# Kernel tuning notes

Measured on AMD Instinct MI355X. Metric: run time of the kernel, lower is better.

## Reference

```python
import jax, jax.numpy as jnp
import numpy as np

B = 524288
IN_DIM = 16
OUT_DIM = 32  # hidden_dim3
N_CHUNKS = 4
CHUNK = 4


def ste_round(x):
    # straight-through round (grad passes unchanged, like Round.apply)
    return x + jax.lax.stop_gradient(jnp.round(x) - x)


def ste_sign(x):
    # straight-through sign (grad passes unchanged, like Sign.apply)
    return x + jax.lax.stop_gradient(jnp.sign(x) - x)


def setup_inputs() -> dict:
    key = jax.random.key(0)
    k1, k2 = jax.random.split(key)
    Input = jax.random.uniform(k1, (B, IN_DIM), dtype=jnp.float32)
    weight = jax.random.normal(k2, (OUT_DIM, IN_DIM), dtype=jnp.float32)
    InMin = jnp.float32(0.0)
    InMax = jnp.float32(1.0)
    return {"Input": Input, "weight": weight, "InMin": InMin, "InMax": InMax}


def reference(Input, weight, InMin, InMax):
    # eval-mode forward of QuantLinear
    scale = InMax - InMin
    w = ste_sign(weight)                       # [O, I] in {-1, 0, 1}
    wP = jax.nn.relu(w)                        # positive mask
    wM = jax.nn.relu(-w)                       # negative mask

    # 4-bit input quantization (eval path): clip(round((x-min)/(max-min)*15), 0, 15)
    q = jnp.clip(ste_round((Input - InMin) / scale * 15.0), 0.0, 15.0)  # [B, I]

    # bias = linear(InMin * ones, w): each row = InMin * sum_j w[o, j]
    bias = InMin * jnp.sum(w, axis=1)          # [O], broadcasts over batch

    # chunked 4-wide linears, vectorized over the 4 chunks
    qc = q.reshape(B, N_CHUNKS, CHUNK)         # [B, C, 4]
    wPc = wP.reshape(OUT_DIM, N_CHUNKS, CHUNK)  # [O, C, 4]
    wMc = wM.reshape(OUT_DIM, N_CHUNKS, CHUNK)
    yP = jnp.einsum('bcf,ocf->cbo', qc, wPc)   # [C, B, O]
    yM = jnp.einsum('bcf,ocf->cbo', qc, wMc)   # [C, B, O]

    # accumulate clip(round(y/15), -4, 4) * (InMax - InMin) over all 8 terms
    terms = jnp.clip(ste_round(yP / 15.0), -4.0, 4.0) \
          + jnp.clip(ste_round(-yM / 15.0), -4.0, 4.0)  # [C, B, O]
    x = jnp.sum(terms, axis=0) * scale + bias  # [B, O]
    return x
```

## Files before the change

### kernel.cpp

```cpp
#include <hip/hip_runtime.h>
#include <stdint.h>


#if __has_builtin(__builtin_amdgcn_sdot4)
#define HAVE_SDOT4 1
#else
#define HAVE_SDOT4 0
#endif

__device__ __forceinline__ int dot7(uint32_t q, uint32_t m) {
#if HAVE_SDOT4
    return __builtin_amdgcn_sdot4((int)q, (int)m, 7, false);
#else
    return (int)(((q & m) * 0x01010101u) >> 24) + 7;
#endif
}

__device__ __forceinline__ int r15(int y7) {
    return (int)(((uint32_t)y7 * 274u) >> 12);
}

__global__ __launch_bounds__(256) void qlin_kernel(
    const float* __restrict__ in, const float* __restrict__ wgt,
    const float* __restrict__ pmin, const float* __restrict__ pmax,
    float* __restrict__ out, int nrows)
{
    __shared__ uint4 smask[64];
    __shared__ __align__(16) float sbias[32];

    const int t = threadIdx.x;
    const int lane = t & 63;
    const int wave = (blockIdx.x << 2) + (t >> 6);
    const size_t R0 = (size_t)wave * 64;

    const float4* inp = (const float4*)in + R0 * 4 + lane;
    float4 f0, f1, f2, f3;
    const bool live = (long)R0 < (long)nrows;
    if (live) {
        f0 = inp[0];
        f1 = inp[64];
        f2 = inp[128];
        f3 = inp[192];
    }

    const float InMin = pmin[0];
    const float InMax = pmax[0];
    const float scale = __fsub_rn(InMax, InMin);

    const uint32_t MASKBYTE = HAVE_SDOT4 ? 1u : 0xFFu;

    {
        int o = t >> 3, k = t & 7, c = k & 3, isM = k >> 2;
        const float* wrow = wgt + o * 16 + c * 4;
        uint32_t m = 0;
#pragma unroll
        for (int j = 0; j < 4; ++j) {
            float v = wrow[j];
            bool sel = isM ? (v < 0.0f) : (v > 0.0f);
            if (sel) m |= MASKBYTE << (8 * j);
        }
        ((uint32_t*)smask)[o * 8 + isM * 4 + c] = m;
    }
    __syncthreads();
    if (t < 32) {
        const uint32_t* mo = (const uint32_t*)smask + t * 8;
        int s = 0;
#pragma unroll
        for (int c = 0; c < 4; ++c)
            s += __popc(mo[c]) - __popc(mo[4 + c]);
        if (!HAVE_SDOT4) s /= 8;
        sbias[t] = __fmul_rn(InMin, (float)s);
    }
    __syncthreads();

    if (!live) return;

    const int ogrp = lane & 7;
    const int rsel = lane >> 3;
    const int srcb = rsel << 2;

    const uint4 MP0 = smask[(ogrp * 4 + 0) * 2], MM0 = smask[(ogrp * 4 + 0) * 2 + 1];
    const uint4 MP1 = smask[(ogrp * 4 + 1) * 2], MM1 = smask[(ogrp * 4 + 1) * 2 + 1];
    const uint4 MP2 = smask[(ogrp * 4 + 2) * 2], MM2 = smask[(ogrp * 4 + 2) * 2 + 1];
    const uint4 MP3 = smask[(ogrp * 4 + 3) * 2], MM3 = smask[(ogrp * 4 + 3) * 2 + 1];
    const float4 bias = *(const float4*)(sbias + ogrp * 4);

    const bool unit = (scale == 1.0f);

#define QUANT(F, QW)                                                        \
    {                                                                       \
        float e[4] = { F.x, F.y, F.z, F.w };                                \
        uint32_t pk = 0;                                                    \
        _Pragma("unroll")                                                   \
        for (int j = 0; j < 4; ++j) {                                       \
            float d  = __fsub_rn(e[j], InMin);                              \
            float sd = unit ? d : __fdiv_rn(d, scale);                      \
            float v  = __fmul_rn(sd, 15.0f);                                \
            float rr = rintf(v);                                            \
            rr = fminf(fmaxf(rr, 0.0f), 15.0f);                             \
            pk |= ((uint32_t)(int)rr) << (8 * j);                           \
        }                                                                   \
        QW = pk;                                                            \
    }

#define ROWCOMP(q0, q1, q2, q3, dst)                                        \
        {                                                                   \
            int a0 = r15(dot7(q0, MP0.x)) - r15(dot7(q0, MM0.x))            \
                   + r15(dot7(q1, MP0.y)) - r15(dot7(q1, MM0.y))            \
                   + r15(dot7(q2, MP0.z)) - r15(dot7(q2, MM0.z))            \
                   + r15(dot7(q3, MP0.w)) - r15(dot7(q3, MM0.w));           \
            int a1 = r15(dot7(q0, MP1.x)) - r15(dot7(q0, MM1.x))            \
                   + r15(dot7(q1, MP1.y)) - r15(dot7(q1, MM1.y))            \
                   + r15(dot7(q2, MP1.z)) - r15(dot7(q2, MM1.z))            \
                   + r15(dot7(q3, MP1.w)) - r15(dot7(q3, MM1.w));           \
            int a2 = r15(dot7(q0, MP2.x)) - r15(dot7(q0, MM2.x))            \
                   + r15(dot7(q1, MP2.y)) - r15(dot7(q1, MM2.y))            \
                   + r15(dot7(q2, MP2.z)) - r15(dot7(q2, MM2.z))            \
                   + r15(dot7(q3, MP2.w)) - r15(dot7(q3, MM2.w));           \
            int a3 = r15(dot7(q0, MP3.x)) - r15(dot7(q0, MM3.x))            \
                   + r15(dot7(q1, MP3.y)) - r15(dot7(q1, MM3.y))            \
                   + r15(dot7(q2, MP3.z)) - r15(dot7(q2, MM3.z))            \
                   + r15(dot7(q3, MP3.w)) - r15(dot7(q3, MM3.w));           \
            float4 res;                                                     \
            res.x = __fadd_rn(__fmul_rn((float)a0, scale), bias.x);         \
            res.y = __fadd_rn(__fmul_rn((float)a1, scale), bias.y);         \
            res.z = __fadd_rn(__fmul_rn((float)a2, scale), bias.z);         \
            res.w = __fadd_rn(__fmul_rn((float)a3, scale), bias.w);         \
            *(float4*)(dst) = res;                                          \
        }

#define SLAB(F, K)                                                          \
    {                                                                       \
        uint32_t qw;                                                        \
        QUANT(F, qw);                                                       \
        const uint32_t qA0 = __shfl(qw, srcb + 0, 64);                      \
        const uint32_t qA1 = __shfl(qw, srcb + 1, 64);                      \
        const uint32_t qA2 = __shfl(qw, srcb + 2, 64);                      \
        const uint32_t qA3 = __shfl(qw, srcb + 3, 64);                      \
        const uint32_t qB0 = __shfl(qw, 32 + srcb + 0, 64);                 \
        const uint32_t qB1 = __shfl(qw, 32 + srcb + 1, 64);                 \
        const uint32_t qB2 = __shfl(qw, 32 + srcb + 2, 64);                 \
        const uint32_t qB3 = __shfl(qw, 32 + srcb + 3, 64);                 \
        float* p0 = out + (R0 + (size_t)(K)*16 + rsel) * 32 + (ogrp << 2);  \
        ROWCOMP(qA0, qA1, qA2, qA3, p0);                                    \
        ROWCOMP(qB0, qB1, qB2, qB3, p0 + 8 * 32);                           \
    }

    SLAB(f0, 0)
    SLAB(f1, 1)
    SLAB(f2, 2)
    SLAB(f3, 3)

#undef SLAB
#undef ROWCOMP
#undef QUANT
}

extern "C" void kernel_launch(void* const* d_in, const int* in_sizes, int n_in,
                              void* d_out, int out_size, void* d_ws, size_t ws_size,
                              hipStream_t stream) {
    (void)n_in; (void)d_ws; (void)ws_size; (void)out_size;
    const float* in  = (const float*)d_in[0];
    const float* wgt = (const float*)d_in[1];
    const float* mn  = (const float*)d_in[2];
    const float* mx  = (const float*)d_in[3];
    float* out = (float*)d_out;
    const int nrows = in_sizes[0] / 16;
    const int blocks = (nrows + 255) / 256;
    qlin_kernel<<<blocks, 256, 0, stream>>>(in, wgt, mn, mx, out, nrows);
}
```

Baseline: 106.3 us.

## Split weight-mask prep into separate kernel; transpose via LDS and nontemporal stores

Moves construction of the weight sign masks and bias into a one-block prep kernel that writes to workspace, so the main kernel no longer needs per-block mask building and two barriers. The main kernel replaces eight cross-lane shuffles per slab with an LDS write plus two vector reads, staggers input loads to reduce register pressure, and writes output with nontemporal stores. It also drops the tail guard and assumes the row count is a multiple of 256, and adds a second kernel launch.

```diff
diff --git a/kernel.cpp b/kernel.cpp
--- a/kernel.cpp
+++ b/kernel.cpp
@@ -7,6 +7,8 @@
 #else
 #define HAVE_SDOT4 0
 #endif
+
+typedef float f32x4 __attribute__((ext_vector_type(4)));
 
 __device__ __forceinline__ int dot7(uint32_t q, uint32_t m) {
 #if HAVE_SDOT4
@@ -20,35 +22,12 @@
     return (int)(((uint32_t)y7 * 274u) >> 12);
 }
 
-__global__ __launch_bounds__(256) void qlin_kernel(
-    const float* __restrict__ in, const float* __restrict__ wgt,
-    const float* __restrict__ pmin, const float* __restrict__ pmax,
-    float* __restrict__ out, int nrows)
+__global__ void qlin_prep(const float* __restrict__ wgt,
+                          const float* __restrict__ pmin,
+                          uint32_t* __restrict__ ws)
 {
-    __shared__ uint4 smask[64];
-    __shared__ __align__(16) float sbias[32];
-
     const int t = threadIdx.x;
-    const int lane = t & 63;
-    const int wave = (blockIdx.x << 2) + (t >> 6);
-    const size_t R0 = (size_t)wave * 64;
-
-    const float4* inp = (const float4*)in + R0 * 4 + lane;
-    float4 f0, f1, f2, f3;
-    const bool live = (long)R0 < (long)nrows;
-    if (live) {
-        f0 = inp[0];
-        f1 = inp[64];
-        f2 = inp[128];
-        f3 = inp[192];
-    }
-
-    const float InMin = pmin[0];
-    const float InMax = pmax[0];
-    const float scale = __fsub_rn(InMax, InMin);
-
     const uint32_t MASKBYTE = HAVE_SDOT4 ? 1u : 0xFFu;
-
     {
         int o = t >> 3, k = t & 7, c = k & 3, isM = k >> 2;
         const float* wrow = wgt + o * 16 + c * 4;
@@ -59,32 +38,50 @@
             bool sel = isM ? (v < 0.0f) : (v > 0.0f);
             if (sel) m |= MASKBYTE << (8 * j);
         }
-        ((uint32_t*)smask)[o * 8 + isM * 4 + c] = m;
+        ws[o * 8 + isM * 4 + c] = m;
     }
-    __syncthreads();
     if (t < 32) {
-        const uint32_t* mo = (const uint32_t*)smask + t * 8;
+        const float* wrow = wgt + t * 16;
         int s = 0;
 #pragma unroll
-        for (int c = 0; c < 4; ++c)
-            s += __popc(mo[c]) - __popc(mo[4 + c]);
-        if (!HAVE_SDOT4) s /= 8;
-        sbias[t] = __fmul_rn(InMin, (float)s);
+        for (int j = 0; j < 16; ++j) {
+            float v = wrow[j];
+            s += (v > 0.0f) ? 1 : 0;
+            s -= (v < 0.0f) ? 1 : 0;
+        }
+        ((float*)ws)[256 + t] = __fmul_rn(pmin[0], (float)s);
     }
-    __syncthreads();
+}
 
-    if (!live) return;
+__global__ __launch_bounds__(256) void qlin_main(
+    const float* __restrict__ in, const uint32_t* __restrict__ ws,
+    const float* __restrict__ pmin, const float* __restrict__ pmax,
+    float* __restrict__ out, int nrows)
+{
+    __shared__ __align__(16) uint32_t xpose[256];
+    const int t = threadIdx.x;
+    const int lane = t & 63;
+    const int wv = t >> 6;
+    const size_t R0 = ((size_t)blockIdx.x * 4 + wv) * 64;
+    (void)nrows;
+
+    const float4* inp = (const float4*)in + R0 * 4 + lane;
+    float4 fa = inp[0];
+    float4 fb = inp[64];
 
     const int ogrp = lane & 7;
     const int rsel = lane >> 3;
-    const int srcb = rsel << 2;
+    uint32_t* xp = xpose + (wv << 6);
 
-    const uint4 MP0 = smask[(ogrp * 4 + 0) * 2], MM0 = smask[(ogrp * 4 + 0) * 2 + 1];
-    const uint4 MP1 = smask[(ogrp * 4 + 1) * 2], MM1 = smask[(ogrp * 4 + 1) * 2 + 1];
-    const uint4 MP2 = smask[(ogrp * 4 + 2) * 2], MM2 = smask[(ogrp * 4 + 2) * 2 + 1];
-    const uint4 MP3 = smask[(ogrp * 4 + 3) * 2], MM3 = smask[(ogrp * 4 + 3) * 2 + 1];
-    const float4 bias = *(const float4*)(sbias + ogrp * 4);
+    const uint4* mw = (const uint4*)ws;
+    const uint4 MP0 = mw[(ogrp * 4 + 0) * 2], MM0 = mw[(ogrp * 4 + 0) * 2 + 1];
+    const uint4 MP1 = mw[(ogrp * 4 + 1) * 2], MM1 = mw[(ogrp * 4 + 1) * 2 + 1];
+    const uint4 MP2 = mw[(ogrp * 4 + 2) * 2], MM2 = mw[(ogrp * 4 + 2) * 2 + 1];
+    const uint4 MP3 = mw[(ogrp * 4 + 3) * 2], MM3 = mw[(ogrp * 4 + 3) * 2 + 1];
+    const float4 bias = ((const float4*)((const float*)ws + 256))[ogrp];
 
+    const float InMin = pmin[0];
+    const float scale = __fsub_rn(pmax[0], InMin);
     const bool unit = (scale == 1.0f);
 
 #define QUANT(F, QW)                                                        \
@@ -94,7 +91,8 @@
         _Pragma("unroll")                                                   \
         for (int j = 0; j < 4; ++j) {                                       \
             float d  = __fsub_rn(e[j], InMin);                              \
-            float sd = unit ? d : __fdiv_rn(d, scale);                      \
+            float sd;                                                       \
+            if (unit) sd = d; else sd = __fdiv_rn(d, scale);                \
             float v  = __fmul_rn(sd, 15.0f);                                \
             float rr = rintf(v);                                            \
             rr = fminf(fmaxf(rr, 0.0f), 15.0f);                             \
@@ -121,35 +119,31 @@
                    + r15(dot7(q1, MP3.y)) - r15(dot7(q1, MM3.y))            \
                    + r15(dot7(q2, MP3.z)) - r15(dot7(q2, MM3.z))            \
                    + r15(dot7(q3, MP3.w)) - r15(dot7(q3, MM3.w));           \
-            float4 res;                                                     \
+            f32x4 res;                                                      \
             res.x = __fadd_rn(__fmul_rn((float)a0, scale), bias.x);         \
             res.y = __fadd_rn(__fmul_rn((float)a1, scale), bias.y);         \
             res.z = __fadd_rn(__fmul_rn((float)a2, scale), bias.z);         \
             res.w = __fadd_rn(__fmul_rn((float)a3, scale), bias.w);         \
-            *(float4*)(dst) = res;                                          \
+            __builtin_nontemporal_store(res, (f32x4*)(dst));                \
         }
 
-#define SLAB(F, K)                                                          \
+#define SLAB(F, K, PRELOAD)                                                 \
     {                                                                       \
         uint32_t qw;                                                        \
         QUANT(F, qw);                                                       \
-        const uint32_t qA0 = __shfl(qw, srcb + 0, 64);                      \
-        const uint32_t qA1 = __shfl(qw, srcb + 1, 64);                      \
-        const uint32_t qA2 = __shfl(qw, srcb + 2, 64);                      \
-        const uint32_t qA3 = __shfl(qw, srcb + 3, 64);                      \
-        const uint32_t qB0 = __shfl(qw, 32 + srcb + 0, 64);                 \
-        const uint32_t qB1 = __shfl(qw, 32 + srcb + 1, 64);                 \
-        const uint32_t qB2 = __shfl(qw, 32 + srcb + 2, 64);                 \
-        const uint32_t qB3 = __shfl(qw, 32 + srcb + 3, 64);                 \
-        float* p0 = out + (R0 + (size_t)(K)*16 + rsel) * 32 + (ogrp << 2);  \
-        ROWCOMP(qA0, qA1, qA2, qA3, p0);                                    \
-        ROWCOMP(qB0, qB1, qB2, qB3, p0 + 8 * 32);                           \
+        xp[lane] = qw;                                                      \
+        PRELOAD                                                             \
+        const uint4 qA = *(const uint4*)(xp + (rsel << 2));                 \
+        const uint4 qB = *(const uint4*)(xp + 32 + (rsel << 2));            \
+        float* p0 = out + (R0 + (size_t)(K) * 16 + rsel) * 32 + (ogrp << 2);\
+        ROWCOMP(qA.x, qA.y, qA.z, qA.w, p0);                                \
+        ROWCOMP(qB.x, qB.y, qB.z, qB.w, p0 + 256);                          \
     }
 
-    SLAB(f0, 0)
-    SLAB(f1, 1)
-    SLAB(f2, 2)
-    SLAB(f3, 3)
+    SLAB(fa, 0, fa = inp[128];)
+    SLAB(fb, 1, fb = inp[192];)
+    SLAB(fa, 2, )
+    SLAB(fb, 3, )
 
 #undef SLAB
 #undef ROWCOMP
@@ -159,13 +153,16 @@
 extern "C" void kernel_launch(void* const* d_in, const int* in_sizes, int n_in,
                               void* d_out, int out_size, void* d_ws, size_t ws_size,
                               hipStream_t stream) {
-    (void)n_in; (void)d_ws; (void)ws_size; (void)out_size;
+    (void)n_in; (void)ws_size; (void)out_size;
     const float* in  = (const float*)d_in[0];
     const float* wgt = (const float*)d_in[1];
     const float* mn  = (const float*)d_in[2];
     const float* mx  = (const float*)d_in[3];
     float* out = (float*)d_out;
+    uint32_t* ws = (uint32_t*)d_ws;
     const int nrows = in_sizes[0] / 16;
-    const int blocks = (nrows + 255) / 256;
-    qlin_kernel<<<blocks, 256, 0, stream>>>(in, wgt, mn, mx, out, nrows);
+    const int blocks = nrows / 256;
+
+    qlin_prep<<<1, 256, 0, stream>>>(wgt, mn, ws);
+    qlin_main<<<blocks, 256, 0, stream>>>(in, ws, mn, mx, out, nrows);
 }
```

Result: no change. 106.8 us (+0.5%).
